# Performance work log

Measured on AMD Instinct MI355X. Metric: run time of the kernel, lower is better.

## Reference

```python
import jax, jax.numpy as jnp
import numpy as np

B, D, H, E, TOPK, NTASK = 16384, 128, 4, 8, 2, 1
ODIM = D // H  # MoE expert output dim (input_feat // num_heads)


def setup_inputs() -> dict:
    key = jax.random.key(0)
    ks = jax.random.split(key, 12)
    s = lambda k, shp, fan: jax.random.normal(k, shp, jnp.float32) / np.sqrt(fan)
    return {
        "x": jax.random.normal(ks[0], (B, D), jnp.float32),
        "Wq": s(ks[1], (D, D * H), D), "bq": jnp.zeros((D * H,), jnp.float32),
        "Wk": s(ks[2], (D, D * H), D), "bk": jnp.zeros((D * H,), jnp.float32),
        "Wg": s(ks[3], (D, E), D),
        "W1": s(ks[4], (E, D, D), D), "b1": jnp.zeros((E, D), jnp.float32),
        "W2": s(ks[5], (E, D, ODIM), D), "b2": jnp.zeros((E, ODIM), jnp.float32),
        "Wout": s(ks[6], (H * ODIM, NTASK), H * ODIM),
        "bout": jnp.zeros((NTASK,), jnp.float32),
    }


def reference(x, Wq, bq, Wk, bk, Wg, W1, b1, W2, b2, Wout, bout):
    # query/key projections -> [B, H, D] token views, flattened to [N, D]
    tok = (x @ Wq + bq).reshape(B * H, D)
    gate_tok = (x @ Wk + bk).reshape(B * H, D)

    # gating: softmax over experts, top-2 routing with renormalized weights
    probs = jax.nn.softmax(gate_tok @ Wg, axis=-1)          # [N, E]
    top_p, top_i = jax.lax.top_k(probs, TOPK)               # [N, k]
    weights = top_p / jnp.sum(top_p, axis=-1, keepdims=True)

    # expert MLPs (dense all-expert compute, then gather selected)
    h = jax.nn.relu(jnp.einsum('nd,edh->neh', tok, W1) + b1)  # [N, E, D]
    eo = jnp.einsum('neh,eho->neo', h, W2) + b2               # [N, E, ODIM]
    sel = jnp.take_along_axis(eo, top_i[:, :, None], axis=1)  # [N, k, ODIM]
    y = jnp.sum(weights[:, :, None] * sel, axis=1)            # [N, ODIM]

    # load-balancing auxiliary loss (switch-style): E * sum(frac_i * mean_prob_i)
    one_hot = jax.nn.one_hot(top_i[:, 0], E, dtype=probs.dtype)
    frac = jnp.mean(one_hot, axis=0)
    mean_p = jnp.mean(probs, axis=0)
    aux_loss = E * jnp.sum(frac * mean_p)

    out = y.reshape(B, H * ODIM) @ Wout + bout                # [B, NTASK]
    return out, aux_loss
```

## Files before the change

kernel.cpp:

```cpp
#include <hip/hip_runtime.h>
#include <hip/hip_bf16.h>

#define BB   16384
#define DD   128
#define HH   4
#define EE   8
#define NN   (BB*HH)
#define OD   32
#define PT   136
#define NL   32
#define CAP2 6144

typedef __attribute__((ext_vector_type(8))) short short8;
typedef __attribute__((ext_vector_type(4))) short short4v;
typedef __attribute__((ext_vector_type(4))) float f32x4;

static __device__ __forceinline__ short f2bf(float v) {
    unsigned int u = __builtin_bit_cast(unsigned int, v);
    u = (u + 0x7FFFu + ((u >> 16) & 1u)) >> 16;
    return (short)u;
}
static __device__ __forceinline__ float bf2f(short b) {
    unsigned int u = ((unsigned int)(unsigned short)b) << 16;
    return __builtin_bit_cast(float, u);
}

__global__ __launch_bounds__(256) void prep2(
    const float* __restrict__ x, const float* __restrict__ Wq, const float* __restrict__ bq,
    const float* __restrict__ Wk, const float* __restrict__ Wg, const float* __restrict__ bk,
    const float* __restrict__ W1, const float* __restrict__ b1, const float* __restrict__ W2,
    const float* __restrict__ bout,
    short* __restrict__ xb, short* __restrict__ A1F, float* __restrict__ bias1,
    short* __restrict__ W2F, float* __restrict__ Wkg, float* __restrict__ bkg,
    float* __restrict__ out, int* __restrict__ cursors)
{
    if (blockIdx.x < 32) {
        __shared__ short L[128 * PT];
        const int li = blockIdx.x;
        const int e = li >> 2, h = li & 3;
        const int t = threadIdx.x;
        const int wv = t >> 6, lane = t & 63, l16 = lane & 15, quad = lane >> 4;

        #pragma unroll
        for (int rep = 0; rep < 16; ++rep) {
            int idx = t + rep * 256;
            int c = idx >> 5, h4 = (idx & 31) * 4;
            float4 v = *(const float4*)(W1 + e * 16384 + c * 128 + h4);
            L[(h4 + 0) * PT + c] = f2bf(v.x);
            L[(h4 + 1) * PT + c] = f2bf(v.y);
            L[(h4 + 2) * PT + c] = f2bf(v.z);
            L[(h4 + 3) * PT + c] = f2bf(v.w);
        }
        __syncthreads();

        short8 af[2][4];
        #pragma unroll
        for (int ml = 0; ml < 2; ++ml)
            #pragma unroll
            for (int ks = 0; ks < 4; ++ks)
                af[ml][ks] = *(const short8*)(L + ((wv*2 + ml)*16 + l16) * PT + ks*32 + quad*8);
        if (t < 128) {
            float s = 0.f;
            #pragma unroll 8
            for (int c = 0; c < 128; ++c)
                s += bq[h*128 + c] * bf2f(L[t * PT + c]);
            bias1[li*128 + t] = s + b1[e*128 + t];
        }
        __syncthreads();

        #pragma unroll
        for (int rep = 0; rep < 4; ++rep) {
            int idx = t + rep * 256;
            int d = idx >> 3, c0 = (idx & 7) * 16;
            const float4* src = (const float4*)(Wq + d * 512 + h * 128 + c0);
            float4 v0 = src[0], v1 = src[1], v2 = src[2], v3 = src[3];
            short8 a, b;
            a[0]=f2bf(v0.x); a[1]=f2bf(v0.y); a[2]=f2bf(v0.z); a[3]=f2bf(v0.w);
            a[4]=f2bf(v1.x); a[5]=f2bf(v1.y); a[6]=f2bf(v1.z); a[7]=f2bf(v1.w);
            b[0]=f2bf(v2.x); b[1]=f2bf(v2.y); b[2]=f2bf(v2.z); b[3]=f2bf(v2.w);
            b[4]=f2bf(v3.x); b[5]=f2bf(v3.y); b[6]=f2bf(v3.z); b[7]=f2bf(v3.w);
            *(short8*)(L + d * PT + c0)     = a;
            *(short8*)(L + d * PT + c0 + 8) = b;
        }
        __syncthreads();

        f32x4 acc[2][8];
        #pragma unroll
        for (int ml = 0; ml < 2; ++ml)
            #pragma unroll
            for (int nt = 0; nt < 8; ++nt)
                acc[ml][nt] = (f32x4){0.f, 0.f, 0.f, 0.f};
        #pragma unroll
        for (int ks = 0; ks < 4; ++ks) {
            short8 bf[8];
            #pragma unroll
            for (int nt = 0; nt < 8; ++nt)
                bf[nt] = *(const short8*)(L + (nt*16 + l16) * PT + ks*32 + quad*8);
            #pragma unroll
            for (int ml = 0; ml < 2; ++ml)
                #pragma unroll
                for (int nt = 0; nt < 8; ++nt)
                    acc[ml][nt] = __builtin_amdgcn_mfma_f32_16x16x32_bf16(af[ml][ks], bf[nt], acc[ml][nt], 0, 0, 0);
        }
        __syncthreads();

        #pragma unroll
        for (int ml = 0; ml < 2; ++ml)
            #pragma unroll
            for (int nt = 0; nt < 8; ++nt)
                #pragma unroll
                for (int r = 0; r < 4; ++r)
                    L[((wv*2 + ml)*16 + quad*4 + r) * PT + nt*16 + l16] = f2bf(acc[ml][nt][r]);
        __syncthreads();

        #pragma unroll
        for (int mt = 0; mt < 8; ++mt)
            #pragma unroll
            for (int ks = 0; ks < 4; ++ks) {
                short8 v = *(const short8*)(L + (mt*16 + l16) * PT + ks*32 + quad*8);
                *(short8*)(A1F + ((size_t)(((li*8 + mt)*4 + ks)*64 + lane)) * 8) = v;
            }
        return;
    }

    int idx = (blockIdx.x - 32) * 256 + threadIdx.x;
    if (idx < 262144) {
        const float4* x4 = (const float4*)x;
        float4 v0 = x4[idx * 2], v1 = x4[idx * 2 + 1];
        short8 s;
        s[0]=f2bf(v0.x); s[1]=f2bf(v0.y); s[2]=f2bf(v0.z); s[3]=f2bf(v0.w);
        s[4]=f2bf(v1.x); s[5]=f2bf(v1.y); s[6]=f2bf(v1.z); s[7]=f2bf(v1.w);
        *(short8*)(xb + (size_t)idx * 8) = s;
    } else if (idx < 294912) {
        int r = idx - 262144;
        int j = r & 7, lane = (r >> 3) & 63, ks = (r >> 9) & 3, mt = (r >> 11) & 1, e = r >> 12;
        int l16 = lane & 15, quad = lane >> 4;
        int m = mt * 16 + l16, k = ks * 32 + quad * 8 + j;
        W2F[r] = f2bf(W2[e * 4096 + k * 32 + m]);
    } else if (idx < 299008) {
        int r = idx - 294912;
        int k = r >> 5, col = r & 31, hh = col >> 3, e = col & 7;
        float s = 0.f;
        #pragma unroll 8
        for (int d = 0; d < 128; ++d) s += Wk[k * 512 + hh * 128 + d] * Wg[d * 8 + e];
        Wkg[k * 32 + col] = s;
    } else if (idx < 299040) {
        int r = idx - 299008;
        int hh = r >> 3, e = r & 7;
        float s = 0.f;
        #pragma unroll 8
        for (int d = 0; d < 128; ++d) s += bk[hh * 128 + d] * Wg[d * 8 + e];
        bkg[r] = s;
    } else if (idx < 315424) {
        out[idx - 299040] = bout[0];
    } else if (idx < 315456) {
        int r = idx - 315424;
        cursors[r] = r * CAP2;
    }
}

__global__ __launch_bounds__(256) void k1_gate(
    const float* __restrict__ x, const float* __restrict__ Wkg, const float* __restrict__ bkg,
    float* __restrict__ wts, float* __restrict__ blkPart,
    int* __restrict__ cursors, int* __restrict__ listIdx)
{
    __shared__ float xL[64 * 129];
    __shared__ float lps[EE];
    __shared__ float lcn[EE];
    __shared__ int   lcnt[NL];
    __shared__ int   lbase[NL];

    const int t  = threadIdx.x;
    const int b0 = blockIdx.x * 64;

    if (t < EE) { lps[t] = 0.f; lcn[t] = 0.f; }
    if (t < NL) lcnt[t] = 0;

    for (int i = t; i < 2048; i += 256) {
        int r = i >> 5, c = i & 31;
        float4 v = ((const float4*)(x + (size_t)(b0 + r) * 128))[c];
        float* dst = xL + r * 129 + c * 4;
        dst[0] = v.x; dst[1] = v.y; dst[2] = v.z; dst[3] = v.w;
    }
    __syncthreads();

    const int h  = __builtin_amdgcn_readfirstlane(t >> 6);
    const int lb = t & 63;

    const f32x4* wkg4 = (const f32x4*)Wkg;
    f32x4 a0 = ((const f32x4*)bkg)[h * 2];
    f32x4 a1 = ((const f32x4*)bkg)[h * 2 + 1];

    const float* xrow = xL + lb * 129;
    #pragma unroll 4
    for (int k = 0; k < 128; ++k) {
        float xv = xrow[k];
        f32x4 w0 = wkg4[k * 8 + h * 2];
        f32x4 w1 = wkg4[k * 8 + h * 2 + 1];
        a0 += w0 * xv;
        a1 += w1 * xv;
    }

    float l[8] = {a0[0], a0[1], a0[2], a0[3], a1[0], a1[1], a1[2], a1[3]};
    float mx = l[0];
    #pragma unroll
    for (int e = 1; e < 8; ++e) mx = fmaxf(mx, l[e]);
    float p[8]; float sm = 0.f;
    #pragma unroll
    for (int e = 0; e < 8; ++e) { p[e] = __expf(l[e] - mx); sm += p[e]; }
    float isin = 1.f / sm;
    #pragma unroll
    for (int e = 0; e < 8; ++e) p[e] *= isin;

    int i1 = 0; float p1 = p[0];
    #pragma unroll
    for (int e = 1; e < 8; ++e) if (p[e] > p1) { p1 = p[e]; i1 = e; }
    int i2 = (i1 == 0) ? 1 : 0; float p2 = p[i2];
    #pragma unroll
    for (int e = 0; e < 8; ++e) if (e != i1 && p[e] > p2) { p2 = p[e]; i2 = e; }

    int n = (b0 + lb) * 4 + h;
    float rinv = 1.f / (p1 + p2);
    wts[2*n]    = p1 * rinv; wts[2*n+1]  = p2 * rinv;

    int li0 = i1 * 4 + h, li1 = i2 * 4 + h;
    int s0 = atomicAdd(&lcnt[li0], 1);
    int s1 = atomicAdd(&lcnt[li1], 1);

    #pragma unroll
    for (int e = 0; e < 8; ++e) {
        float v = p[e];
        #pragma unroll
        for (int m2 = 1; m2 < 64; m2 <<= 1) v += __shfl_xor(v, m2);
        unsigned long long m1b = __ballot(i1 == e);
        if (lb == 0) {
            atomicAdd(&lps[e], v);
            atomicAdd(&lcn[e], (float)__popcll(m1b));
        }
    }
    __syncthreads();
    if (t < NL) lbase[t] = atomicAdd(&cursors[t], lcnt[t]);
    __syncthreads();

    int q0 = lbase[li0] + s0;
    if (q0 < (li0 + 1) * CAP2) listIdx[q0] = 2*n;
    int q1 = lbase[li1] + s1;
    if (q1 < (li1 + 1) * CAP2) listIdx[q1] = 2*n + 1;

    if (t < EE) {
        float* bp = blkPart + blockIdx.x * 16;
        bp[t]     = lps[t];
        bp[8 + t] = lcn[t];
    }
}

__global__ __launch_bounds__(256) void k2b_expert(
    const short* __restrict__ xb, const short* __restrict__ A1F,
    const float* __restrict__ bias1, const short* __restrict__ W2F, const float* __restrict__ b2,
    const int* __restrict__ cursors, const int* __restrict__ listIdx,
    const float* __restrict__ wts, const float* __restrict__ Wout,
    const float* __restrict__ blkPart, float* __restrict__ out)
{
    __shared__ short tokL[64 * PT];
    __shared__ short hL[64 * PT];
    __shared__ int   ids[64];
    __shared__ float wsl[64];
    __shared__ float red[16][16];
    __shared__ float fin[16];

    const int li = blockIdx.y;
    const int e  = li >> 2;
    const int h  = li & 3;
    const int t  = threadIdx.x;

    if (blockIdx.x == gridDim.x - 1 && li == NL - 1) {
        int chunk = t >> 4, col = t & 15;
        float v = 0.f;
        for (int i = 0; i < 16; ++i) v += blkPart[(chunk * 16 + i) * 16 + col];
        red[chunk][col] = v;
        __syncthreads();
        if (t < 16) {
            float s = 0.f;
            #pragma unroll
            for (int c = 0; c < 16; ++c) s += red[c][t];
            fin[t] = s;
        }
        __syncthreads();
        if (t == 0) {
            float aux = 0.f;
            const float invN = 1.f / (float)NN;
            for (int e2 = 0; e2 < EE; ++e2) aux += (fin[8 + e2] * invN) * (fin[e2] * invN);
            out[BB] = (float)EE * aux;
        }
    }

    int cnt = cursors[li] - li * CAP2;
    if (cnt > CAP2) cnt = CAP2;
    const int off = blockIdx.x * 64;
    if (off >= cnt) return;
    const int sb  = li * CAP2 + off;
    const int nt  = min(64, cnt - off);

    if (t < 64) {
        int a = listIdx[sb + min(t, nt - 1)];
        ids[t] = a >> 3;
        wsl[t] = (t < nt) ? wts[a] : 0.f;
    }
    __syncthreads();

    #pragma unroll
    for (int r = 0; r < 4; ++r) {
        int i = t + r * 256;
        int slot = i >> 4, seg = i & 15;
        short8 v = *(const short8*)(xb + (size_t)ids[slot] * 128 + seg * 8);
        *(short8*)(tokL + slot * PT + seg * 8) = v;
    }
    __syncthreads();

    const int wv   = t >> 6;
    const int lane = t & 63;
    const int l16  = lane & 15;
    const int quad = lane >> 4;

    f32x4 acc[2][4];
    #pragma unroll
    for (int ml = 0; ml < 2; ++ml)
        #pragma unroll
        for (int nl = 0; nl < 4; ++nl)
            acc[ml][nl] = (f32x4){0.f, 0.f, 0.f, 0.f};

    short8 af[2][4];
    #pragma unroll
    for (int ml = 0; ml < 2; ++ml)
        #pragma unroll
        for (int ks = 0; ks < 4; ++ks)
            af[ml][ks] = *(const short8*)(A1F + ((size_t)(((li*8 + wv*2 + ml)*4 + ks)*64 + lane)) * 8);

    short8 bf[4][4];
    #pragma unroll
    for (int nl = 0; nl < 4; ++nl)
        #pragma unroll
        for (int ks = 0; ks < 4; ++ks)
            bf[nl][ks] = *(const short8*)(tokL + (nl*16 + l16) * PT + ks*32 + quad*8);

    #pragma unroll
    for (int ks = 0; ks < 4; ++ks)
        #pragma unroll
        for (int ml = 0; ml < 2; ++ml)
            #pragma unroll
            for (int nl = 0; nl < 4; ++nl)
                acc[ml][nl] = __builtin_amdgcn_mfma_f32_16x16x32_bf16(af[ml][ks], bf[nl][ks], acc[ml][nl], 0, 0, 0);

    #pragma unroll
    for (int ml = 0; ml < 2; ++ml) {
        int hid0 = wv*32 + ml*16 + quad*4;
        f32x4 b1v = *(const f32x4*)(bias1 + li*128 + hid0);
        #pragma unroll
        for (int nl = 0; nl < 4; ++nl) {
            short4v hv;
            #pragma unroll
            for (int r = 0; r < 4; ++r) {
                float v = acc[ml][nl][r] + b1v[r];
                hv[r] = f2bf(fmaxf(v, 0.f));
            }
            *(short4v*)(hL + (nl*16 + l16) * PT + hid0) = hv;
        }
    }
    __syncthreads();

    f32x4 acc2[2];
    acc2[0] = (f32x4){0.f, 0.f, 0.f, 0.f};
    acc2[1] = (f32x4){0.f, 0.f, 0.f, 0.f};

    short8 af2[2][4];
    #pragma unroll
    for (int ml = 0; ml < 2; ++ml)
        #pragma unroll
        for (int ks = 0; ks < 4; ++ks)
            af2[ml][ks] = *(const short8*)(W2F + ((size_t)(((e*2 + ml)*4 + ks)*64 + lane)) * 8);

    short8 bf2[4];
    #pragma unroll
    for (int ks = 0; ks < 4; ++ks)
        bf2[ks] = *(const short8*)(hL + (wv*16 + l16) * PT + ks*32 + quad*8);

    #pragma unroll
    for (int ks = 0; ks < 4; ++ks)
        #pragma unroll
        for (int ml = 0; ml < 2; ++ml)
            acc2[ml] = __builtin_amdgcn_mfma_f32_16x16x32_bf16(af2[ml][ks], bf2[ks], acc2[ml], 0, 0, 0);

    const int slot = wv*16 + l16;
    const int b    = ids[slot];
    float partial = 0.f;
    #pragma unroll
    for (int ml = 0; ml < 2; ++ml) {
        int od0 = ml*16 + quad*4;
        f32x4 b2v = *(const f32x4*)(b2 + e*32 + od0);
        f32x4 wv4 = *(const f32x4*)(Wout + h*32 + od0);
        #pragma unroll
        for (int r = 0; r < 4; ++r)
            partial += (acc2[ml][r] + b2v[r]) * wv4[r];
    }
    partial += __shfl_xor(partial, 16);
    partial += __shfl_xor(partial, 32);
    if (quad == 0) {
        float v = partial * wsl[slot];
        atomicAdd(&out[b], v);
    }
}

extern "C" void kernel_launch(void* const* d_in, const int* in_sizes, int n_in,
                              void* d_out, int out_size, void* d_ws, size_t ws_size,
                              hipStream_t stream) {
    (void)in_sizes; (void)n_in; (void)out_size; (void)ws_size;
    const float* x    = (const float*)d_in[0];
    const float* Wq   = (const float*)d_in[1];
    const float* bq   = (const float*)d_in[2];
    const float* Wk   = (const float*)d_in[3];
    const float* bk   = (const float*)d_in[4];
    const float* Wg   = (const float*)d_in[5];
    const float* W1   = (const float*)d_in[6];
    const float* b1   = (const float*)d_in[7];
    const float* W2   = (const float*)d_in[8];
    const float* b2   = (const float*)d_in[9];
    const float* Wout = (const float*)d_in[10];
    const float* bout = (const float*)d_in[11];
    float* out = (float*)d_out;

    char* ws = (char*)d_ws;
    short* xb       = (short*)(ws + 0);
    float* wts      = (float*)(ws + 4194304);
    int*   listIdx  = (int*)  (ws + 4718592);
    short* A1F      = (short*)(ws + 5505024);
    short* W2F      = (short*)(ws + 6553600);
    float* Wkg      = (float*)(ws + 6619136);
    float* bkg      = (float*)(ws + 6635520);
    float* bias1    = (float*)(ws + 6635648);
    float* blkPart  = (float*)(ws + 6652032);
    int*   cursors  = (int*)  (ws + 6668416);

    prep2<<<1265, 256, 0, stream>>>(x, Wq, bq, Wk, Wg, bk, W1, b1, W2, bout,
                                    xb, A1F, bias1, W2F, Wkg, bkg, out, cursors);
    k1_gate<<<256, 256, 0, stream>>>(x, Wkg, bkg, wts, blkPart, cursors, listIdx);
    k2b_expert<<<dim3(CAP2/64, NL), 256, 0, stream>>>(xb, A1F, bias1, W2F, b2,
                                    cursors, listIdx, wts, Wout, blkPart, out);
}
```

Before: 131.9 us.

## Split tiny prep kernel and fuse gating with weight/input conversion

Moves the small Wkg/bkg precompute, output init and cursor reset into a tiny first kernel. The gating pass, the W1·Wq fold, the x-to-bf16 conversion and the W2 repacking then run as different block ranges of one combined kernel. This lets the gating work run alongside the heavy prep work instead of waiting behind it, and the conversion blocks use a grid-stride loop. It still needs three launches, and the combined kernel reserves the larger shared-memory footprint for every block, which may lower occupancy.

```diff
diff --git a/kernel.cpp b/kernel.cpp
--- a/kernel.cpp
+++ b/kernel.cpp
@@ -25,20 +25,138 @@
     return __builtin_bit_cast(float, u);
 }
 
-__global__ __launch_bounds__(256) void prep2(
-    const float* __restrict__ x, const float* __restrict__ Wq, const float* __restrict__ bq,
-    const float* __restrict__ Wk, const float* __restrict__ Wg, const float* __restrict__ bk,
-    const float* __restrict__ W1, const float* __restrict__ b1, const float* __restrict__ W2,
-    const float* __restrict__ bout,
-    short* __restrict__ xb, short* __restrict__ A1F, float* __restrict__ bias1,
-    short* __restrict__ W2F, float* __restrict__ Wkg, float* __restrict__ bkg,
+__global__ __launch_bounds__(256) void prep_tiny(
+    const float* __restrict__ Wk, const float* __restrict__ Wg,
+    const float* __restrict__ bk, const float* __restrict__ bout,
+    float* __restrict__ Wkg, float* __restrict__ bkg,
     float* __restrict__ out, int* __restrict__ cursors)
 {
-    if (blockIdx.x < 32) {
-        __shared__ short L[128 * PT];
-        const int li = blockIdx.x;
+    int idx = blockIdx.x * 256 + threadIdx.x;
+    if (idx < 4096) {
+        int k = idx >> 5, col = idx & 31, hh = col >> 3, e = col & 7;
+        float s = 0.f;
+        #pragma unroll 8
+        for (int d = 0; d < 128; ++d) s += Wk[k * 512 + hh * 128 + d] * Wg[d * 8 + e];
+        Wkg[k * 32 + col] = s;
+    } else if (idx < 4128) {
+        int r = idx - 4096;
+        int hh = r >> 3, e = r & 7;
+        float s = 0.f;
+        #pragma unroll 8
+        for (int d = 0; d < 128; ++d) s += bk[hh * 128 + d] * Wg[d * 8 + e];
+        bkg[r] = s;
+    } else if (idx < 20512) {
+        out[idx - 4128] = bout[0];
+    } else if (idx < 20544) {
+        int r = idx - 20512;
+        cursors[r] = r * CAP2;
+    }
+}
+
+__global__ __launch_bounds__(256) void mid(
+    const float* __restrict__ x, const float* __restrict__ Wq, const float* __restrict__ bq,
+    const float* __restrict__ W1, const float* __restrict__ b1, const float* __restrict__ W2,
+    const float* __restrict__ Wkg, const float* __restrict__ bkg,
+    short* __restrict__ xb, short* __restrict__ A1F, float* __restrict__ bias1,
+    short* __restrict__ W2F, float* __restrict__ wts, float* __restrict__ blkPart,
+    int* __restrict__ cursors, int* __restrict__ listIdx)
+{
+    __shared__ __align__(16) char smemU[34816];
+    __shared__ float lps[EE];
+    __shared__ float lcn[EE];
+    __shared__ int   lcnt[NL];
+    __shared__ int   lbase[NL];
+
+    const int blk = blockIdx.x;
+    const int t   = threadIdx.x;
+
+    if (blk < 256) {
+        float* xL = (float*)smemU;
+        const int b0 = blk * 64;
+
+        if (t < EE) { lps[t] = 0.f; lcn[t] = 0.f; }
+        if (t < NL) lcnt[t] = 0;
+
+        for (int i = t; i < 2048; i += 256) {
+            int r = i >> 5, c = i & 31;
+            float4 v = ((const float4*)(x + (size_t)(b0 + r) * 128))[c];
+            float* dst = xL + r * 129 + c * 4;
+            dst[0] = v.x; dst[1] = v.y; dst[2] = v.z; dst[3] = v.w;
+        }
+        __syncthreads();
+
+        const int h  = __builtin_amdgcn_readfirstlane(t >> 6);
+        const int lb = t & 63;
+
+        const f32x4* wkg4 = (const f32x4*)Wkg;
+        f32x4 a0 = ((const f32x4*)bkg)[h * 2];
+        f32x4 a1 = ((const f32x4*)bkg)[h * 2 + 1];
+
+        const float* xrow = xL + lb * 129;
+        #pragma unroll 4
+        for (int k = 0; k < 128; ++k) {
+            float xv = xrow[k];
+            f32x4 w0 = wkg4[k * 8 + h * 2];
+            f32x4 w1 = wkg4[k * 8 + h * 2 + 1];
+            a0 += w0 * xv;
+            a1 += w1 * xv;
+        }
+
+        float l[8] = {a0[0], a0[1], a0[2], a0[3], a1[0], a1[1], a1[2], a1[3]};
+        float mx = l[0];
+        #pragma unroll
+        for (int e = 1; e < 8; ++e) mx = fmaxf(mx, l[e]);
+        float p[8]; float sm = 0.f;
+        #pragma unroll
+        for (int e = 0; e < 8; ++e) { p[e] = __expf(l[e] - mx); sm += p[e]; }
+        float isin = 1.f / sm;
+        #pragma unroll
+        for (int e = 0; e < 8; ++e) p[e] *= isin;
+
+        int i1 = 0; float p1 = p[0];
+        #pragma unroll
+        for (int e = 1; e < 8; ++e) if (p[e] > p1) { p1 = p[e]; i1 = e; }
+        int i2 = (i1 == 0) ? 1 : 0; float p2 = p[i2];
+        #pragma unroll
+        for (int e = 0; e < 8; ++e) if (e != i1 && p[e] > p2) { p2 = p[e]; i2 = e; }
+
+        int n = (b0 + lb) * 4 + h;
+        float rinv = 1.f / (p1 + p2);
+        wts[2*n]    = p1 * rinv; wts[2*n+1]  = p2 * rinv;
+
+        int li0 = i1 * 4 + h, li1 = i2 * 4 + h;
+        int s0 = atomicAdd(&lcnt[li0], 1);
+        int s1 = atomicAdd(&lcnt[li1], 1);
+
+        #pragma unroll
+        for (int e = 0; e < 8; ++e) {
+            float v = p[e];
+            #pragma unroll
+            for (int m2 = 1; m2 < 64; m2 <<= 1) v += __shfl_xor(v, m2);
+            unsigned long long m1b = __ballot(i1 == e);
+            if (lb == 0) {
+                atomicAdd(&lps[e], v);
+                atomicAdd(&lcn[e], (float)__popcll(m1b));
+            }
+        }
+        __syncthreads();
+        if (t < NL) lbase[t] = atomicAdd(&cursors[t], lcnt[t]);
+        __syncthreads();
+
+        int q0 = lbase[li0] + s0;
+        if (q0 < (li0 + 1) * CAP2) listIdx[q0] = 2*n;
+        int q1 = lbase[li1] + s1;
+        if (q1 < (li1 + 1) * CAP2) listIdx[q1] = 2*n + 1;
+
+        if (t < EE) {
+            float* bp = blkPart + blk * 16;
+            bp[t]     = lps[t];
+            bp[8 + t] = lcn[t];
+        }
+    } else if (blk < 288) {
+        short* L = (short*)smemU;
+        const int li = blk - 256;
         const int e = li >> 2, h = li & 3;
-        const int t = threadIdx.x;
         const int wv = t >> 6, lane = t & 63, l16 = lane & 15, quad = lane >> 4;
 
         #pragma unroll
@@ -88,29 +206,29 @@
         #pragma unroll
         for (int ml = 0; ml < 2; ++ml)
             #pragma unroll
-            for (int nt = 0; nt < 8; ++nt)
-                acc[ml][nt] = (f32x4){0.f, 0.f, 0.f, 0.f};
+            for (int nt2 = 0; nt2 < 8; ++nt2)
+                acc[ml][nt2] = (f32x4){0.f, 0.f, 0.f, 0.f};
         #pragma unroll
         for (int ks = 0; ks < 4; ++ks) {
-            short8 bf[8];
-            #pragma unroll
-            for (int nt = 0; nt < 8; ++nt)
-                bf[nt] = *(const short8*)(L + (nt*16 + l16) * PT + ks*32 + quad*8);
+            short8 bfr[8];
+            #pragma unroll
+            for (int nt2 = 0; nt2 < 8; ++nt2)
+                bfr[nt2] = *(const short8*)(L + (nt2*16 + l16) * PT + ks*32 + quad*8);
             #pragma unroll
             for (int ml = 0; ml < 2; ++ml)
                 #pragma unroll
-                for (int nt = 0; nt < 8; ++nt)
-                    acc[ml][nt] = __builtin_amdgcn_mfma_f32_16x16x32_bf16(af[ml][ks], bf[nt], acc[ml][nt], 0, 0, 0);
+                for (int nt2 = 0; nt2 < 8; ++nt2)
+                    acc[ml][nt2] = __builtin_amdgcn_mfma_f32_16x16x32_bf16(af[ml][ks], bfr[nt2], acc[ml][nt2], 0, 0, 0);
         }
         __syncthreads();
 
         #pragma unroll
         for (int ml = 0; ml < 2; ++ml)
             #pragma unroll
-            for (int nt = 0; nt < 8; ++nt)
+            for (int nt2 = 0; nt2 < 8; ++nt2)
                 #pragma unroll
                 for (int r = 0; r < 4; ++r)
-                    L[((wv*2 + ml)*16 + quad*4 + r) * PT + nt*16 + l16] = f2bf(acc[ml][nt][r]);
+                    L[((wv*2 + ml)*16 + quad*4 + r) * PT + nt2*16 + l16] = f2bf(acc[ml][nt2][r]);
         __syncthreads();
 
         #pragma unroll
@@ -120,137 +238,24 @@
                 short8 v = *(const short8*)(L + (mt*16 + l16) * PT + ks*32 + quad*8);
                 *(short8*)(A1F + ((size_t)(((li*8 + mt)*4 + ks)*64 + lane)) * 8) = v;
             }
-        return;
-    }
-
-    int idx = (blockIdx.x - 32) * 256 + threadIdx.x;
-    if (idx < 262144) {
-        const float4* x4 = (const float4*)x;
-        float4 v0 = x4[idx * 2], v1 = x4[idx * 2 + 1];
-        short8 s;
-        s[0]=f2bf(v0.x); s[1]=f2bf(v0.y); s[2]=f2bf(v0.z); s[3]=f2bf(v0.w);
-        s[4]=f2bf(v1.x); s[5]=f2bf(v1.y); s[6]=f2bf(v1.z); s[7]=f2bf(v1.w);
-        *(short8*)(xb + (size_t)idx * 8) = s;
-    } else if (idx < 294912) {
-        int r = idx - 262144;
-        int j = r & 7, lane = (r >> 3) & 63, ks = (r >> 9) & 3, mt = (r >> 11) & 1, e = r >> 12;
-        int l16 = lane & 15, quad = lane >> 4;
-        int m = mt * 16 + l16, k = ks * 32 + quad * 8 + j;
-        W2F[r] = f2bf(W2[e * 4096 + k * 32 + m]);
-    } else if (idx < 299008) {
-        int r = idx - 294912;
-        int k = r >> 5, col = r & 31, hh = col >> 3, e = col & 7;
-        float s = 0.f;
-        #pragma unroll 8
-        for (int d = 0; d < 128; ++d) s += Wk[k * 512 + hh * 128 + d] * Wg[d * 8 + e];
-        Wkg[k * 32 + col] = s;
-    } else if (idx < 299040) {
-        int r = idx - 299008;
-        int hh = r >> 3, e = r & 7;
-        float s = 0.f;
-        #pragma unroll 8
-        for (int d = 0; d < 128; ++d) s += bk[hh * 128 + d] * Wg[d * 8 + e];
-        bkg[r] = s;
-    } else if (idx < 315424) {
-        out[idx - 299040] = bout[0];
-    } else if (idx < 315456) {
-        int r = idx - 315424;
-        cursors[r] = r * CAP2;
-    }
-}
-
-__global__ __launch_bounds__(256) void k1_gate(
-    const float* __restrict__ x, const float* __restrict__ Wkg, const float* __restrict__ bkg,
-    float* __restrict__ wts, float* __restrict__ blkPart,
-    int* __restrict__ cursors, int* __restrict__ listIdx)
-{
-    __shared__ float xL[64 * 129];
-    __shared__ float lps[EE];
-    __shared__ float lcn[EE];
-    __shared__ int   lcnt[NL];
-    __shared__ int   lbase[NL];
-
-    const int t  = threadIdx.x;
-    const int b0 = blockIdx.x * 64;
-
-    if (t < EE) { lps[t] = 0.f; lcn[t] = 0.f; }
-    if (t < NL) lcnt[t] = 0;
-
-    for (int i = t; i < 2048; i += 256) {
-        int r = i >> 5, c = i & 31;
-        float4 v = ((const float4*)(x + (size_t)(b0 + r) * 128))[c];
-        float* dst = xL + r * 129 + c * 4;
-        dst[0] = v.x; dst[1] = v.y; dst[2] = v.z; dst[3] = v.w;
-    }
-    __syncthreads();
-
-    const int h  = __builtin_amdgcn_readfirstlane(t >> 6);
-    const int lb = t & 63;
-
-    const f32x4* wkg4 = (const f32x4*)Wkg;
-    f32x4 a0 = ((const f32x4*)bkg)[h * 2];
-    f32x4 a1 = ((const f32x4*)bkg)[h * 2 + 1];
-
-    const float* xrow = xL + lb * 129;
-    #pragma unroll 4
-    for (int k = 0; k < 128; ++k) {
-        float xv = xrow[k];
-        f32x4 w0 = wkg4[k * 8 + h * 2];
-        f32x4 w1 = wkg4[k * 8 + h * 2 + 1];
-        a0 += w0 * xv;
-        a1 += w1 * xv;
-    }
-
-    float l[8] = {a0[0], a0[1], a0[2], a0[3], a1[0], a1[1], a1[2], a1[3]};
-    float mx = l[0];
-    #pragma unroll
-    for (int e = 1; e < 8; ++e) mx = fmaxf(mx, l[e]);
-    float p[8]; float sm = 0.f;
-    #pragma unroll
-    for (int e = 0; e < 8; ++e) { p[e] = __expf(l[e] - mx); sm += p[e]; }
-    float isin = 1.f / sm;
-    #pragma unroll
-    for (int e = 0; e < 8; ++e) p[e] *= isin;
-
-    int i1 = 0; float p1 = p[0];
-    #pragma unroll
-    for (int e = 1; e < 8; ++e) if (p[e] > p1) { p1 = p[e]; i1 = e; }
-    int i2 = (i1 == 0) ? 1 : 0; float p2 = p[i2];
-    #pragma unroll
-    for (int e = 0; e < 8; ++e) if (e != i1 && p[e] > p2) { p2 = p[e]; i2 = e; }
-
-    int n = (b0 + lb) * 4 + h;
-    float rinv = 1.f / (p1 + p2);
-    wts[2*n]    = p1 * rinv; wts[2*n+1]  = p2 * rinv;
-
-    int li0 = i1 * 4 + h, li1 = i2 * 4 + h;
-    int s0 = atomicAdd(&lcnt[li0], 1);
-    int s1 = atomicAdd(&lcnt[li1], 1);
-
-    #pragma unroll
-    for (int e = 0; e < 8; ++e) {
-        float v = p[e];
-        #pragma unroll
-        for (int m2 = 1; m2 < 64; m2 <<= 1) v += __shfl_xor(v, m2);
-        unsigned long long m1b = __ballot(i1 == e);
-        if (lb == 0) {
-            atomicAdd(&lps[e], v);
-            atomicAdd(&lcn[e], (float)__popcll(m1b));
-        }
-    }
-    __syncthreads();
-    if (t < NL) lbase[t] = atomicAdd(&cursors[t], lcnt[t]);
-    __syncthreads();
-
-    int q0 = lbase[li0] + s0;
-    if (q0 < (li0 + 1) * CAP2) listIdx[q0] = 2*n;
-    int q1 = lbase[li1] + s1;
-    if (q1 < (li1 + 1) * CAP2) listIdx[q1] = 2*n + 1;
-
-    if (t < EE) {
-        float* bp = blkPart + blockIdx.x * 16;
-        bp[t]     = lps[t];
-        bp[8 + t] = lcn[t];
+    } else {
+        for (int s = blk - 288; s < 1152; s += 896) {
+            if (s < 1024) {
+                int idx = s * 256 + t;
+                const float4* x4 = (const float4*)x;
+                float4 v0 = x4[idx * 2], v1 = x4[idx * 2 + 1];
+                short8 sv;
+                sv[0]=f2bf(v0.x); sv[1]=f2bf(v0.y); sv[2]=f2bf(v0.z); sv[3]=f2bf(v0.w);
+                sv[4]=f2bf(v1.x); sv[5]=f2bf(v1.y); sv[6]=f2bf(v1.z); sv[7]=f2bf(v1.w);
+                *(short8*)(xb + (size_t)idx * 8) = sv;
+            } else {
+                int r = (s - 1024) * 256 + t;
+                int j = r & 7, lane = (r >> 3) & 63, ks = (r >> 9) & 3, mt = (r >> 11) & 1, e = r >> 12;
+                int l16 = lane & 15, quad = lane >> 4;
+                int m = mt * 16 + l16, k = ks * 32 + quad * 8 + j;
+                W2F[r] = f2bf(W2[e * 4096 + k * 32 + m]);
+            }
+        }
     }
 }
 
@@ -336,12 +341,12 @@
         for (int ks = 0; ks < 4; ++ks)
             af[ml][ks] = *(const short8*)(A1F + ((size_t)(((li*8 + wv*2 + ml)*4 + ks)*64 + lane)) * 8);
 
-    short8 bf[4][4];
+    short8 bfr[4][4];
     #pragma unroll
     for (int nl = 0; nl < 4; ++nl)
         #pragma unroll
         for (int ks = 0; ks < 4; ++ks)
-            bf[nl][ks] = *(const short8*)(tokL + (nl*16 + l16) * PT + ks*32 + quad*8);
+            bfr[nl][ks] = *(const short8*)(tokL + (nl*16 + l16) * PT + ks*32 + quad*8);
 
     #pragma unroll
     for (int ks = 0; ks < 4; ++ks)
@@ -349,7 +354,7 @@
         for (int ml = 0; ml < 2; ++ml)
             #pragma unroll
             for (int nl = 0; nl < 4; ++nl)
-                acc[ml][nl] = __builtin_amdgcn_mfma_f32_16x16x32_bf16(af[ml][ks], bf[nl][ks], acc[ml][nl], 0, 0, 0);
+                acc[ml][nl] = __builtin_amdgcn_mfma_f32_16x16x32_bf16(af[ml][ks], bfr[nl][ks], acc[ml][nl], 0, 0, 0);
 
     #pragma unroll
     for (int ml = 0; ml < 2; ++ml) {
@@ -440,9 +445,9 @@
     float* blkPart  = (float*)(ws + 6652032);
     int*   cursors  = (int*)  (ws + 6668416);
 
-    prep2<<<1265, 256, 0, stream>>>(x, Wq, bq, Wk, Wg, bk, W1, b1, W2, bout,
-                                    xb, A1F, bias1, W2F, Wkg, bkg, out, cursors);
-    k1_gate<<<256, 256, 0, stream>>>(x, Wkg, bkg, wts, blkPart, cursors, listIdx);
-    k2b_expert<<<dim3(CAP2/64, NL), 256, 0, stream>>>(xb, A1F, bias1, W2F, b2,
-                                    cursors, listIdx, wts, Wout, blkPart, out);
-}
+    prep_tiny<<<81, 256, 0, stream>>>(Wk, Wg, bk, bout, Wkg, bkg, out, cursors);
+    mid<<<1184, 256, 0, stream>>>(x, Wq, bq, W1, b1, W2, Wkg, bkg,
+                                  xb, A1F, bias1, W2F, wts, blkPart, cursors, listIdx);
+    k2b_expert<<<dim3(96, NL), 256, 0, stream>>>(xb, A1F, bias1, W2F, b2,
+                                  cursors, listIdx, wts, Wout, blkPart, out);
+}
```

Result: faster. 126.5 us (-4.1%).
